# Kernel optimization log

Measured on AMD Instinct MI355X. Metric: run time of the kernel, lower is better.

Reference implementation:

```python
import jax, jax.numpy as jnp
import numpy as np

N_HEADS = 16


def setup_inputs() -> dict:
    key = jax.random.key(0)
    k1, k2, k3 = jax.random.split(key, 3)
    d = 1024
    x = jax.random.normal(k1, (8, 1024, d), dtype=jnp.float32)
    w_qkv = jax.random.normal(k2, (d, 3 * d), dtype=jnp.float32) * (1.0 / np.sqrt(d))
    w_out = jax.random.normal(k3, (d, d), dtype=jnp.float32) * (1.0 / np.sqrt(d))
    b_out = jnp.zeros((d,), dtype=jnp.float32)
    return {"x": x, "w_qkv": w_qkv, "w_out": w_out, "b_out": b_out}


def reference(x, w_qkv, w_out, b_out):
    a, b, c = x.shape
    h = N_HEADS
    hd = c // h
    scale = 1.0 / (c ** 0.5)  # note: 1/sqrt(model_dim), not head_dim
    qkv = (x @ w_qkv).reshape(a, b, 3, h, hd)
    q, k, v = jnp.moveaxis(qkv, 2, 0)          # each (a, b, h, hd)
    q = jnp.swapaxes(q, 1, 2)                  # (a, h, b, hd)
    k = jnp.swapaxes(k, 1, 2)
    v = jnp.swapaxes(v, 1, 2)
    scores = jnp.einsum('ahqd,ahkd->ahqk', q, k) * scale  # (a, h, b, b)
    # Faithful to the source: softmax over dim=1 (the HEADS axis)
    attn = jax.nn.softmax(scores, axis=1)
    out = jnp.einsum('ahqk,ahkd->ahqd', attn, v)           # (a, h, b, hd)
    out = jnp.swapaxes(out, 1, 2).reshape(a, b, c)
    return out @ w_out + b_out
```

## Files before the change

### kernel.cpp

```cpp
#include <hip/hip_runtime.h>
#include <hip/hip_bf16.h>

typedef __attribute__((ext_vector_type(8))) short short8;
typedef __attribute__((ext_vector_type(4))) float f32x4;
typedef __attribute__((ext_vector_type(16))) float f32x16;
typedef __attribute__((ext_vector_type(4))) unsigned uint4v;

#define SC_LOG2E 0.04508422f
#define MFMA32(a, b, c) __builtin_amdgcn_mfma_f32_32x32x16_bf16(a, b, c, 0, 0, 0)

__device__ inline short bf16r(float f) {
    union { float f; unsigned u; } v; v.f = f;
    unsigned r = v.u + 0x7FFFu + ((v.u >> 16) & 1u);
    return (short)(r >> 16);
}
__device__ inline float bflo(unsigned u) {
    union { unsigned u; float f; } v; v.u = u << 16; return v.f;
}
__device__ inline float bfhi(unsigned u) {
    union { unsigned u; float f; } v; v.u = u & 0xffff0000u; return v.f;
}
__device__ inline unsigned cvt_pk_bf16(float lo, float hi) {
    unsigned r;
    asm("v_cvt_pk_bf16_f32 %0, %1, %2" : "=v"(r) : "v"(lo), "v"(hi));
    return r;
}
__device__ inline void perm32swap(unsigned& a, unsigned& b) {
    asm("v_permlane32_swap_b32 %0, %1" : "+v"(a), "+v"(b));
}

#define GLOAD_LDS16(gp, lp) __builtin_amdgcn_global_load_lds( \
    (const __attribute__((address_space(1))) unsigned int*)(gp), \
    (__attribute__((address_space(3))) unsigned int*)(lp), 16, 0, 0)

__global__ void castk(const float* __restrict__ in, short* __restrict__ out, int n4) {
    int i = blockIdx.x * 256 + threadIdx.x;
    if (i < n4) {
        float4 v = ((const float4*)in)[i];
        short4 o;
        o.x = bf16r(v.x); o.y = bf16r(v.y); o.z = bf16r(v.z); o.w = bf16r(v.w);
        ((short4*)out)[i] = o;
    }
}

__global__ void tcast(const float* __restrict__ src, short* __restrict__ dst, int R, int C,
                      int nscale, float sfac) {
    __shared__ float tile[32][33];
    int bi = blockIdx.x, bj = blockIdx.y;
    int tx = threadIdx.x & 31, ty = threadIdx.x >> 5;
#pragma unroll
    for (int p = 0; p < 4; p++)
        tile[ty + p * 8][tx] = src[(long)(bi * 32 + ty + p * 8) * C + bj * 32 + tx];
    __syncthreads();
#pragma unroll
    for (int p = 0; p < 4; p++) {
        int n = bj * 32 + ty + p * 8;
        float v = tile[tx][ty + p * 8];
        if (n < nscale) v *= sfac;
        dst[(long)n * R + bi * 32 + tx] = bf16r(v);
    }
}

__global__ void vtrans(const short* __restrict__ qkv, short* __restrict__ Vt) {
    __shared__ short tile[32][33];
    int a = blockIdx.z, bi = blockIdx.x, bj = blockIdx.y;
    int tx = threadIdx.x & 31, ty = threadIdx.x >> 5;
#pragma unroll
    for (int p = 0; p < 4; p++) {
        int k = bi * 32 + ty + p * 8;
        int r = bj * 32 + tx;
        tile[ty + p * 8][tx] = qkv[(long)(a * 1024 + k) * 3072 + 2048 + r];
    }
    __syncthreads();
#pragma unroll
    for (int p = 0; p < 4; p++) {
        int r = bj * 32 + ty + p * 8;
        int k = bi * 32 + tx;
        Vt[(long)a * 1048576 + (long)r * 1024 + k] = tile[tx][ty + p * 8];
    }
}

template<int OUT_BF16>
__global__ __launch_bounds__(256, 2)
void gemm_bt(const short* __restrict__ A, const short* __restrict__ Bt,
             void* __restrict__ Cout, const float* __restrict__ bias,
             int M, int N, int K, int nbx, int cpx, int lda) {
    __shared__ short As[2][128 * 32];
    __shared__ short Bs[2][128 * 32];
    const int wg = blockIdx.x;
    const int lg = (wg & 7) * cpx + (wg >> 3);
    const int bx = lg % nbx, by = lg / nbx;
    const int tid = threadIdx.x, w = tid >> 6, lane = tid & 63;
    const int wr = w >> 1, wc = w & 1;
    const int l15 = lane & 15, lhi = lane >> 4;
    const int m0 = by * 128, n0 = bx * 128;
    f32x4 acc[4][4] = {};
    const int NT = K / 32;

    auto stage = [&](int buf, int t) {
        int k0 = t * 32;
#pragma unroll
        for (int j = 0; j < 2; j++) {
            int chunk = w * 128 + j * 64 + lane;
            int row = chunk >> 2, cc = chunk & 3;
            GLOAD_LDS16(A  + (long)(m0 + row) * lda + k0 + cc * 8, &As[buf][chunk * 8]);
            GLOAD_LDS16(Bt + (long)(n0 + row) * K   + k0 + cc * 8, &Bs[buf][chunk * 8]);
        }
    };

    stage(0, 0);
    __syncthreads();
    int buf = 0;
    for (int t = 0; t < NT; t++) {
        if (t + 1 < NT) stage(buf ^ 1, t + 1);
        short8 af[4], bfr[4];
#pragma unroll
        for (int i = 0; i < 4; i++) {
            af[i]  = *(const short8*)(&As[buf][(wr * 64 + i * 16 + l15) * 32 + lhi * 8]);
            bfr[i] = *(const short8*)(&Bs[buf][(wc * 64 + i * 16 + l15) * 32 + lhi * 8]);
        }
#pragma unroll
        for (int i = 0; i < 4; i++)
#pragma unroll
            for (int j = 0; j < 4; j++)
                acc[i][j] = __builtin_amdgcn_mfma_f32_16x16x32_bf16(af[i], bfr[j], acc[i][j], 0, 0, 0);
        __syncthreads();
        buf ^= 1;
    }
#pragma unroll
    for (int i = 0; i < 4; i++)
#pragma unroll
        for (int j = 0; j < 4; j++)
#pragma unroll
            for (int r = 0; r < 4; r++) {
                int row = m0 + wr * 64 + i * 16 + lhi * 4 + r;
                int col = n0 + wc * 64 + j * 16 + l15;
                float v = acc[i][j][r];
                if (OUT_BF16) ((short*)Cout)[(long)row * N + col] = bf16r(v);
                else          ((float*)Cout)[(long)row * N + col] = v + bias[col];
            }
}

__global__ __launch_bounds__(256, 2)
void dsum_kernel(const short* __restrict__ qkv, unsigned* __restrict__ negL) {
    __shared__ short Qs[2][128 * 64];
    __shared__ short Ks[2][128 * 64];
    const int wg = blockIdx.x;
    const int lg = (wg & 7) * 64 + (wg >> 3);
    const int a = lg >> 6, q0 = ((lg >> 3) & 7) * 128, k0 = (lg & 7) * 128;
    const int tid = threadIdx.x, w = tid >> 6, lane = tid & 63;
    const int wr = w >> 1, wc = w & 1;
    const int l31 = lane & 31, hi = lane >> 5;
    const long qb = (long)a * 3145728;
    f32x16 dacc[2][2] = {};

    auto stage = [&](int buf, int hh) {
#pragma unroll
        for (int j = 0; j < 4; j++) {
            int c = j * 256 + tid;
            int row = c >> 3, cc = (c & 7) ^ (row & 7);
            GLOAD_LDS16(qkv + qb + (long)(q0 + row) * 3072 + hh * 64 + cc * 8,        &Qs[buf][c * 8]);
            GLOAD_LDS16(qkv + qb + (long)(k0 + row) * 3072 + 1024 + hh * 64 + cc * 8, &Ks[buf][c * 8]);
        }
    };

    stage(0, 0);
    __syncthreads();
    int buf = 0;
    for (int hh = 0; hh < 16; hh++) {
        if (hh < 15) stage(buf ^ 1, hh + 1);
        short8 ka[2][4], qf[2][4];
#pragma unroll
        for (int i = 0; i < 2; i++)
#pragma unroll
            for (int dc = 0; dc < 4; dc++) {
                int row = wr * 64 + i * 32 + l31;
                int ph = (dc * 2 + hi) ^ (row & 7);
                ka[i][dc] = *(const short8*)(&Ks[buf][row * 64 + ph * 8]);
            }
#pragma unroll
        for (int j = 0; j < 2; j++)
#pragma unroll
            for (int dc = 0; dc < 4; dc++) {
                int row = wc * 64 + j * 32 + l31;
                int ph = (dc * 2 + hi) ^ (row & 7);
                qf[j][dc] = *(const short8*)(&Qs[buf][row * 64 + ph * 8]);
            }
#pragma unroll
        for (int i = 0; i < 2; i++)
#pragma unroll
            for (int j = 0; j < 2; j++) {
                f32x16 s = {};
#pragma unroll
                for (int dc = 0; dc < 4; dc++)
                    s = MFMA32(ka[i][dc], qf[j][dc], s);
#pragma unroll
                for (int r = 0; r < 16; r++)
                    dacc[i][j][r] += exp2f(s[r]);
            }
        __syncthreads();
        buf ^= 1;
    }
#pragma unroll
    for (int i = 0; i < 2; i++)
#pragma unroll
        for (int j = 0; j < 2; j++) {
            int ktg = (k0 >> 5) + wr * 2 + i;
            int qtg = (q0 >> 5) + wc * 2 + j;
            unsigned pwv[8];
#pragma unroll
            for (int u = 0; u < 8; u++)
                pwv[u] = cvt_pk_bf16(-__log2f(dacc[i][j][2 * u]),
                                     -__log2f(dacc[i][j][2 * u + 1]));
            unsigned* dst = negL + (((long)(a * 32 + ktg) * 32 + qtg) << 9) + lane * 8;
            *(uint4v*)dst       = (uint4v){pwv[0], pwv[1], pwv[2], pwv[3]};
            *(uint4v*)(dst + 4) = (uint4v){pwv[4], pwv[5], pwv[6], pwv[7]};
        }
}

__global__ __launch_bounds__(256, 2)
void attn2_kernel(const short* __restrict__ qkv, const short* __restrict__ Vt,
                  const unsigned* __restrict__ negL, short* __restrict__ ctx) {
    __shared__ short lds[4 * 8192];
    const int wg = blockIdx.x;
    const int lg = (wg & 7) * 64 + (wg >> 3);
    const int a = lg >> 6, h = (lg >> 2) & 15, qblk = lg & 3;
    const int tid = threadIdx.x, w = tid >> 6, lane = tid & 63;
    const int l31 = lane & 31, hi = lane >> 5;
    const int qw = qblk * 256 + w * 64;
    const long qb = (long)a * 3145728;
    short* Kw = &lds[w * 8192];
    short* Vw = &lds[w * 8192 + 4096];

    short8 qfrag[2][4];
#pragma unroll
    for (int qs = 0; qs < 2; qs++)
#pragma unroll
        for (int dc = 0; dc < 4; dc++)
            qfrag[qs][dc] = *(const short8*)(qkv + qb +
                (long)(qw + qs * 32 + l31) * 3072 + h * 64 + dc * 16 + hi * 8);

    const short* kcol  = qkv + qb + 1024 + h * 64;
    const short* vbase = Vt + (long)a * 1048576 + (long)(h * 64) * 1024;
    const unsigned* lbase = negL + (long)a * 524288 + (qw >> 5) * 512 + lane * 8;

    auto stage = [&](int buf, int t) {
        int k0 = t * 32;
#pragma unroll
        for (int p = 0; p < 4; p++)
            GLOAD_LDS16(kcol + (long)(k0 + l31) * 3072 + p * 16 + hi * 8,
                        Kw + buf * 2048 + (p * 64 + lane) * 8);
#pragma unroll
        for (int p = 0; p < 4; p++) {
            int n = p >> 1, dt = p & 1;
            GLOAD_LDS16(vbase + (long)(dt * 32 + l31) * 1024 + k0 + n * 16 + hi * 8,
                        Vw + buf * 2048 + (p * 64 + lane) * 8);
        }
    };

    f32x16 oacc[2][2] = {};
    stage(0, 0);
    uint4v dmC[2][2];
#pragma unroll
    for (int qs = 0; qs < 2; qs++) {
        dmC[qs][0] = *(const uint4v*)(lbase + qs * 512);
        dmC[qs][1] = *(const uint4v*)(lbase + qs * 512 + 4);
    }

    int buf = 0;
    for (int t = 0; t < 32; t++) {
        stage(buf ^ 1, (t + 1) & 31);
        uint4v dmN[2][2];
#pragma unroll
        for (int qs = 0; qs < 2; qs++) {
            const unsigned* dp = lbase + ((t + 1) & 31) * 16384 + qs * 512;
            dmN[qs][0] = *(const uint4v*)dp;
            dmN[qs][1] = *(const uint4v*)(dp + 4);
        }
        asm volatile("s_waitcnt vmcnt(12)" ::: "memory");
        __builtin_amdgcn_sched_barrier(0);

        short8 ka[4];
#pragma unroll
        for (int dc = 0; dc < 4; dc++)
            ka[dc] = *(const short8*)(Kw + buf * 2048 + (dc * 64 + lane) * 8);

        short8 pfrag[2][2];
#pragma unroll
        for (int qs = 0; qs < 2; qs++) {
            f32x16 s = {};
#pragma unroll
            for (int dc = 0; dc < 4; dc++)
                s = MFMA32(ka[dc], qfrag[qs][dc], s);
            unsigned pw[8];
#pragma unroll
            for (int u = 0; u < 8; u++) {
                unsigned d = dmC[qs][u >> 2][u & 3];
                float e0 = exp2f(s[2 * u]     + bflo(d));
                float e1 = exp2f(s[2 * u + 1] + bfhi(d));
                pw[u] = cvt_pk_bf16(e0, e1);
            }
            perm32swap(pw[0], pw[2]); perm32swap(pw[1], pw[3]);
            perm32swap(pw[4], pw[6]); perm32swap(pw[5], pw[7]);
            union { uint4v u; short8 s8; } c0, c1;
            c0.u = (uint4v){pw[0], pw[1], pw[2], pw[3]};
            c1.u = (uint4v){pw[4], pw[5], pw[6], pw[7]};
            pfrag[qs][0] = c0.s8;
            pfrag[qs][1] = c1.s8;
        }
#pragma unroll
        for (int dt = 0; dt < 2; dt++)
#pragma unroll
            for (int n = 0; n < 2; n++) {
                short8 vf = *(const short8*)(Vw + buf * 2048 + ((n * 2 + dt) * 64 + lane) * 8);
#pragma unroll
                for (int qs = 0; qs < 2; qs++)
                    oacc[qs][dt] = MFMA32(pfrag[qs][n], vf, oacc[qs][dt]);
            }
#pragma unroll
        for (int qs = 0; qs < 2; qs++) {
            dmC[qs][0] = dmN[qs][0];
            dmC[qs][1] = dmN[qs][1];
        }
        buf ^= 1;
    }
#pragma unroll
    for (int qs = 0; qs < 2; qs++)
#pragma unroll
        for (int dt = 0; dt < 2; dt++)
#pragma unroll
            for (int r = 0; r < 16; r++) {
                int q = qw + qs * 32 + (r & 3) + 8 * (r >> 2) + 4 * hi;
                int col = h * 64 + dt * 32 + l31;
                ctx[((long)a * 1024 + q) * 3072 + col] = bf16r(oacc[qs][dt][r]);
            }
}

extern "C" void kernel_launch(void* const* d_in, const int* in_sizes, int n_in,
                              void* d_out, int out_size, void* d_ws, size_t ws_size,
                              hipStream_t stream) {
    const float* x     = (const float*)d_in[0];
    const float* w_qkv = (const float*)d_in[1];
    const float* w_out = (const float*)d_in[2];
    const float* b_out = (const float*)d_in[3];
    float* out = (float*)d_out;

    char* ws = (char*)d_ws;
    short* wqkvT   = (short*)(ws);
    unsigned* negL = (unsigned*)(ws);
    short* woT   = (short*)(ws + 33554432);
    short* qkv   = (short*)(ws + 35651584);
    short* Vt    = (short*)(ws + 85983232);
    short* xb    = (short*)(ws + 85983232);
    short* ctx   = qkv + 2048;
    if (ws_size < 109051904u) return;

    castk<<<8192, 256, 0, stream>>>(x, xb, 2097152);
    tcast<<<dim3(32, 96), 256, 0, stream>>>(w_qkv, wqkvT, 1024, 3072, 1024, SC_LOG2E);
    tcast<<<dim3(32, 32), 256, 0, stream>>>(w_out, woT, 1024, 1024, 0, 1.0f);
    gemm_bt<1><<<1536, 256, 0, stream>>>(xb, wqkvT, (void*)qkv, nullptr, 8192, 3072, 1024, 24, 192, 1024);
    vtrans<<<dim3(32, 32, 8), 256, 0, stream>>>(qkv, Vt);
    dsum_kernel<<<512, 256, 0, stream>>>(qkv, negL);
    attn2_kernel<<<512, 256, 0, stream>>>(qkv, Vt, negL, ctx);
    gemm_bt<0><<<512, 256, 0, stream>>>(ctx, woT, (void*)out, b_out, 8192, 1024, 1024, 8, 64, 3072);
}
```

Baseline: 238.3 us.

## Share K/V tiles across waves with a triple-buffered 64-key LDS pipeline

```diff
diff --git a/kernel.cpp b/kernel.cpp
--- a/kernel.cpp
+++ b/kernel.cpp
@@ -221,7 +221,7 @@
 __global__ __launch_bounds__(256, 2)
 void attn2_kernel(const short* __restrict__ qkv, const short* __restrict__ Vt,
                   const unsigned* __restrict__ negL, short* __restrict__ ctx) {
-    __shared__ short lds[4 * 8192];
+    __shared__ short lds[3 * 8192];
     const int wg = blockIdx.x;
     const int lg = (wg & 7) * 64 + (wg >> 3);
     const int a = lg >> 6, h = (lg >> 2) & 15, qblk = lg & 3;
@@ -229,8 +229,6 @@
     const int l31 = lane & 31, hi = lane >> 5;
     const int qw = qblk * 256 + w * 64;
     const long qb = (long)a * 3145728;
-    short* Kw = &lds[w * 8192];
-    short* Vw = &lds[w * 8192 + 4096];
 
     short8 qfrag[2][4];
 #pragma unroll
@@ -245,84 +243,86 @@
     const unsigned* lbase = negL + (long)a * 524288 + (qw >> 5) * 512 + lane * 8;
 
     auto stage = [&](int buf, int t) {
-        int k0 = t * 32;
-#pragma unroll
-        for (int p = 0; p < 4; p++)
-            GLOAD_LDS16(kcol + (long)(k0 + l31) * 3072 + p * 16 + hi * 8,
-                        Kw + buf * 2048 + (p * 64 + lane) * 8);
-#pragma unroll
-        for (int p = 0; p < 4; p++) {
-            int n = p >> 1, dt = p & 1;
+        int k0 = t * 64;
+#pragma unroll
+        for (int j = 0; j < 2; j++) {
+            GLOAD_LDS16(kcol + (long)(k0 + j * 32 + l31) * 3072 + w * 16 + hi * 8,
+                        &lds[buf * 8192 + (j * 256 + tid) * 8]);
+            int fidx = j * 4 + w, n = fidx >> 1, dt = fidx & 1;
             GLOAD_LDS16(vbase + (long)(dt * 32 + l31) * 1024 + k0 + n * 16 + hi * 8,
-                        Vw + buf * 2048 + (p * 64 + lane) * 8);
+                        &lds[buf * 8192 + 4096 + (j * 256 + tid) * 8]);
         }
     };
 
     f32x16 oacc[2][2] = {};
     stage(0, 0);
-    uint4v dmC[2][2];
-#pragma unroll
-    for (int qs = 0; qs < 2; qs++) {
-        dmC[qs][0] = *(const uint4v*)(lbase + qs * 512);
-        dmC[qs][1] = *(const uint4v*)(lbase + qs * 512 + 4);
-    }
-
-    int buf = 0;
-    for (int t = 0; t < 32; t++) {
-        stage(buf ^ 1, (t + 1) & 31);
-        uint4v dmN[2][2];
-#pragma unroll
-        for (int qs = 0; qs < 2; qs++) {
-            const unsigned* dp = lbase + ((t + 1) & 31) * 16384 + qs * 512;
-            dmN[qs][0] = *(const uint4v*)dp;
-            dmN[qs][1] = *(const uint4v*)(dp + 4);
-        }
-        asm volatile("s_waitcnt vmcnt(12)" ::: "memory");
+    stage(1, 1);
+    asm volatile("s_waitcnt vmcnt(4)\ns_barrier" ::: "memory");
+    __builtin_amdgcn_sched_barrier(0);
+
+    int bR = 0, bW = 2;
+    for (int t = 0; t < 16; t++) {
+        uint4v dm[2][2][2];
+#pragma unroll
+        for (int qs = 0; qs < 2; qs++)
+#pragma unroll
+            for (int kt = 0; kt < 2; kt++) {
+                const unsigned* dp = lbase + (long)(t * 2 + kt) * 16384 + qs * 512;
+                dm[qs][kt][0] = *(const uint4v*)dp;
+                dm[qs][kt][1] = *(const uint4v*)(dp + 4);
+            }
+        if (t + 2 < 16) stage(bW, t + 2);
+
+        const short* Kb = &lds[bR * 8192];
+        const short* Vb = &lds[bR * 8192 + 4096];
+#pragma unroll
+        for (int kt = 0; kt < 2; kt++) {
+            short8 ka[4];
+#pragma unroll
+            for (int dc = 0; dc < 4; dc++)
+                ka[dc] = *(const short8*)(Kb + ((kt * 4 + dc) * 64 + lane) * 8);
+
+            short8 pf[2][2];
+#pragma unroll
+            for (int qs = 0; qs < 2; qs++) {
+                f32x16 s = {};
+                __builtin_amdgcn_s_setprio(1);
+#pragma unroll
+                for (int dc = 0; dc < 4; dc++)
+                    s = MFMA32(ka[dc], qfrag[qs][dc], s);
+                __builtin_amdgcn_s_setprio(0);
+                unsigned pw[8];
+#pragma unroll
+                for (int u = 0; u < 8; u++) {
+                    unsigned d = dm[qs][kt][u >> 2][u & 3];
+                    float e0 = exp2f(s[2 * u]     + bflo(d));
+                    float e1 = exp2f(s[2 * u + 1] + bfhi(d));
+                    pw[u] = cvt_pk_bf16(e0, e1);
+                }
+                perm32swap(pw[0], pw[2]); perm32swap(pw[1], pw[3]);
+                perm32swap(pw[4], pw[6]); perm32swap(pw[5], pw[7]);
+                union { uint4v u; short8 s8; } c0, c1;
+                c0.u = (uint4v){pw[0], pw[1], pw[2], pw[3]};
+                c1.u = (uint4v){pw[4], pw[5], pw[6], pw[7]};
+                pf[qs][0] = c0.s8;
+                pf[qs][1] = c1.s8;
+            }
+            __builtin_amdgcn_s_setprio(1);
+#pragma unroll
+            for (int dt = 0; dt < 2; dt++)
+#pragma unroll
+                for (int nn = 0; nn < 2; nn++) {
+                    short8 vf = *(const short8*)(Vb + (((kt * 2 + nn) * 2 + dt) * 64 + lane) * 8);
+#pragma unroll
+                    for (int qs = 0; qs < 2; qs++)
+                        oacc[qs][dt] = MFMA32(pf[qs][nn], vf, oacc[qs][dt]);
+                }
+            __builtin_amdgcn_s_setprio(0);
+        }
+        asm volatile("s_waitcnt vmcnt(4)\ns_barrier" ::: "memory");
         __builtin_amdgcn_sched_barrier(0);
-
-        short8 ka[4];
-#pragma unroll
-        for (int dc = 0; dc < 4; dc++)
-            ka[dc] = *(const short8*)(Kw + buf * 2048 + (dc * 64 + lane) * 8);
-
-        short8 pfrag[2][2];
-#pragma unroll
-        for (int qs = 0; qs < 2; qs++) {
-            f32x16 s = {};
-#pragma unroll
-            for (int dc = 0; dc < 4; dc++)
-                s = MFMA32(ka[dc], qfrag[qs][dc], s);
-            unsigned pw[8];
-#pragma unroll
-            for (int u = 0; u < 8; u++) {
-                unsigned d = dmC[qs][u >> 2][u & 3];
-                float e0 = exp2f(s[2 * u]     + bflo(d));
-                float e1 = exp2f(s[2 * u + 1] + bfhi(d));
-                pw[u] = cvt_pk_bf16(e0, e1);
-            }
-            perm32swap(pw[0], pw[2]); perm32swap(pw[1], pw[3]);
-            perm32swap(pw[4], pw[6]); perm32swap(pw[5], pw[7]);
-            union { uint4v u; short8 s8; } c0, c1;
-            c0.u = (uint4v){pw[0], pw[1], pw[2], pw[3]};
-            c1.u = (uint4v){pw[4], pw[5], pw[6], pw[7]};
-            pfrag[qs][0] = c0.s8;
-            pfrag[qs][1] = c1.s8;
-        }
-#pragma unroll
-        for (int dt = 0; dt < 2; dt++)
-#pragma unroll
-            for (int n = 0; n < 2; n++) {
-                short8 vf = *(const short8*)(Vw + buf * 2048 + ((n * 2 + dt) * 64 + lane) * 8);
-#pragma unroll
-                for (int qs = 0; qs < 2; qs++)
-                    oacc[qs][dt] = MFMA32(pfrag[qs][n], vf, oacc[qs][dt]);
-            }
-#pragma unroll
-        for (int qs = 0; qs < 2; qs++) {
-            dmC[qs][0] = dmN[qs][0];
-            dmC[qs][1] = dmN[qs][1];
-        }
-        buf ^= 1;
+        bR = (bR == 2) ? 0 : bR + 1;
+        bW = (bW == 2) ? 0 : bW + 1;
     }
 #pragma unroll
     for (int qs = 0; qs < 2; qs++)
```

Result: faster. 227.8 us (-4.4%).
